# Optimization experiments

Measured on AMD Instinct MI355X. Metric: run time of the kernel, lower is better.

The kernel has to match this reference:

```python
import jax, jax.numpy as jnp
import numpy as np

HID = 512
HEADS = 8
D = HID // HEADS          # att_size = 64
B = 64                    # number of graphs
L = 1024                  # bonds per graph (equal-length scopes)
SCALE = D ** (-0.5)
EPS = 1e-5


def setup_inputs() -> dict:
    key = jax.random.key(0)
    ks = jax.random.split(key, 9)
    f = lambda k, s, sc=1.0: jax.random.normal(k, s, dtype=jnp.float32) * sc
    edge_attr = f(ks[0], (B * L, HID))
    # contiguous equal-length scopes: (start, length) per graph
    scopes = np.stack([np.arange(B, dtype=np.int64) * L,
                       np.full(B, L, dtype=np.int64)], axis=1)
    return {
        "edge_attr": edge_attr,
        "batch_scopes": jnp.asarray(scopes),
        "Wq": f(ks[1], (HID, HID), 0.03),   # torch Linear weight [out, in]
        "Wk": f(ks[2], (HID, HID), 0.03),
        "Wv": f(ks[3], (HID, HID), 0.03),
        "Wr": f(ks[4], (D, D), 0.1),
        "w_alpha": f(ks[5], (D,)),
        "w_beta": f(ks[6], (D,)),
        "Wo": f(ks[7], (HID, HID), 0.03),
        "bo": jnp.zeros((HID,), jnp.float32),
        "ln_g": jnp.ones((HID,), jnp.float32),
        "ln_b": jnp.zeros((HID,), jnp.float32),
    }


def reference(edge_attr, batch_scopes, Wq, Wk, Wv, Wr, w_alpha, w_beta,
              Wo, bo, ln_g, ln_b):
    # Scopes are contiguous, equal length L -> pad_sequence == reshape
    padded = edge_attr.reshape(B, L, HID)

    def proj(W):  # (B, L, HID) @ W.T -> (B, heads, L, D)
        return jnp.einsum('blh,dh->bld', padded, W).reshape(B, L, HEADS, D).transpose(0, 2, 1, 3)

    b_q = proj(Wq)
    b_k = proj(Wk)
    b_v = proj(Wv)

    # softmax over the head-feature dim (faithful to dim=-1 in torch code)
    alpha = jax.nn.softmax(b_q * w_alpha * SCALE, axis=-1)
    global_q = jnp.sum(alpha * b_q, axis=2)            # (B, heads, D), sum over L

    p = global_q[:, :, None, :] * b_k                  # (B, heads, L, D)
    beta = jax.nn.softmax(p * w_beta * SCALE, axis=-1)
    global_k = jnp.sum(beta * p, axis=2)               # (B, heads, D)

    kv = global_k[:, :, None, :] * b_v                 # (B, heads, L, D)
    kv_out = jnp.einsum('bhld,ed->bhle', kv, Wr)
    att = jax.nn.relu(kv_out + b_q)                    # dropout p=0 (eval)

    att = att.transpose(0, 2, 1, 3).reshape(B, L, HID)
    out = jnp.einsum('blh,oh->blo', att, Wo) + bo

    # LayerNorm over last dim
    mu = jnp.mean(out, axis=-1, keepdims=True)
    var = jnp.mean((out - mu) ** 2, axis=-1, keepdims=True)
    out = (out - mu) * jax.lax.rsqrt(var + EPS) * ln_g + ln_b

    # unpad + concat == flatten for equal-length contiguous scopes
    return out.reshape(B * L, HID)
```

## Files before the change

kernel.cpp:

```cpp
#include <hip/hip_runtime.h>
#include <stdint.h>


#define SCALE_F 0.125f
#define EPSF 1e-5f

typedef __attribute__((ext_vector_type(8))) short short8;
typedef __attribute__((ext_vector_type(4))) float float4v;
typedef unsigned short ushort_t;

__device__ __forceinline__ ushort_t f2bf(float f) {
  uint32_t u = __builtin_bit_cast(uint32_t, f);
  u += 0x7fffu + ((u >> 16) & 1u);
  return (ushort_t)(u >> 16);
}
__device__ __forceinline__ float bf2f(ushort_t s) {
  uint32_t u = ((uint32_t)s) << 16;
  return __builtin_bit_cast(float, u);
}

__device__ __forceinline__ void gload16(const void* g, void* l) {
  __builtin_amdgcn_global_load_lds(
      (__attribute__((address_space(1))) char*)(char*)const_cast<void*>(g),
      (__attribute__((address_space(3))) char*)(char*)l, 16, 0, 0);
}

#define BARR() asm volatile("s_barrier" ::: "memory")
#define LGKM0() do { asm volatile("s_waitcnt lgkmcnt(0)" ::: "memory"); \
                     __builtin_amdgcn_sched_barrier(0); } while (0)

__global__ __launch_bounds__(256) void cvt_x(const float* __restrict__ X,
                                             ushort_t* __restrict__ Xb) {
  const int i = blockIdx.x * 256 + threadIdx.x;
  const float4v* src = (const float4v*)X;
  float4v v0 = src[(size_t)i * 2];
  float4v v1 = src[(size_t)i * 2 + 1];
  short8 o;
#pragma unroll
  for (int j = 0; j < 4; ++j) {
    o[j]     = (short)f2bf(v0[j]);
    o[j + 4] = (short)f2bf(v1[j]);
  }
  ((short8*)Xb)[i] = o;
}

__global__ __launch_bounds__(256) void cvt_w(const float* __restrict__ Wq,
                                             const float* __restrict__ Wk,
                                             const float* __restrict__ Wv,
                                             const float* __restrict__ Wo,
                                             ushort_t* __restrict__ Wqkv,
                                             ushort_t* __restrict__ Wob) {
  const int i = blockIdx.x * 256 + threadIdx.x;
  if (i < 262144)        Wqkv[i] = f2bf(Wq[i]);
  else if (i < 524288)   Wqkv[i] = f2bf(Wk[i - 262144]);
  else if (i < 786432)   Wqkv[i] = f2bf(Wv[i - 524288]);
  else                   Wob[i - 786432] = f2bf(Wo[i - 786432]);
}

__global__ __launch_bounds__(512, 2) void gemm8p(const ushort_t* __restrict__ A,
                                                 const ushort_t* __restrict__ Bm,
                                                 ushort_t* __restrict__ C) {
  __shared__ __align__(16) char ldsA[65536];
  __shared__ __align__(16) char ldsB[65536];
  const int swz = (blockIdx.x & 7) * 192 + (blockIdx.x >> 3);
  const int tm = swz / 6, tn = swz % 6;
  const int row0 = tm * 256, col0 = tn * 256;
  const int tid = threadIdx.x, wid = tid >> 6, lane = tid & 63;
  const int wr = wid >> 2, wc = wid & 3;
  const int lr = lane & 15, lk = lane >> 4;
  const int xr = (lr & 7) << 4;

  auto stageA = [&](int kt, int h) {
    const int slot = (2 * kt + h) & 3;
    const int rowbase = row0 + h * 128;
#pragma unroll
    for (int i = 0; i < 2; ++i) {
      const int o = i * 8192 + wid * 1024 + lane * 16;
      const int r = o >> 7, x = o & 127;
      gload16((const char*)A + (size_t)(rowbase + r) * 1024 + kt * 128 + (x ^ ((r & 7) << 4)),
              ldsA + slot * 16384 + i * 8192 + wid * 1024);
    }
  };
  auto stageB = [&](int kt, int h) {
    const int slot = (2 * kt + h) & 3;
    const int rowbase = col0 + h * 128;
#pragma unroll
    for (int i = 0; i < 2; ++i) {
      const int o = i * 8192 + wid * 1024 + lane * 16;
      const int r = o >> 7, x = o & 127;
      gload16((const char*)Bm + (size_t)(rowbase + r) * 1024 + kt * 128 + (x ^ ((r & 7) << 4)),
              ldsB + slot * 16384 + i * 8192 + wid * 1024);
    }
  };
  auto rdA = [&](int t, int mi, int kk) -> short8 {
    const int slot = (2 * t + wr) & 3;
    return *(const short8*)(ldsA + slot * 16384 + (mi * 16 + lr) * 128 +
                            ((kk * 64 + lk * 16) ^ xr));
  };
  auto rdB = [&](int t, int ni, int kk) -> short8 {
    const int slot = (2 * t + (wc >> 1)) & 3;
    return *(const short8*)(ldsB + slot * 16384 + ((wc & 1) * 64 + ni * 16 + lr) * 128 +
                            ((kk * 64 + lk * 16) ^ xr));
  };

  float4v acc[8][4] = {};

  stageA(0, 0); stageA(0, 1); stageB(0, 0); stageB(0, 1);
  stageA(1, 0); stageA(1, 1); stageB(1, 0);
  asm volatile("s_waitcnt vmcnt(6)" ::: "memory");
  BARR();

#pragma unroll
  for (int t = 0; t < 8; ++t) {
    short8 a0[4][2], a1[4][2], b0[2][2], b1[2][2];
#pragma unroll
    for (int mi = 0; mi < 4; ++mi)
#pragma unroll
      for (int kk = 0; kk < 2; ++kk) a0[mi][kk] = rdA(t, mi, kk);
#pragma unroll
    for (int ni = 0; ni < 2; ++ni)
#pragma unroll
      for (int kk = 0; kk < 2; ++kk) b0[ni][kk] = rdB(t, ni, kk);
    if (t + 1 < 8) stageB(t + 1, 1);
    BARR();
    LGKM0();
    __builtin_amdgcn_s_setprio(1);
#pragma unroll
    for (int kk = 0; kk < 2; ++kk)
#pragma unroll
      for (int mi = 0; mi < 4; ++mi)
#pragma unroll
        for (int ni = 0; ni < 2; ++ni)
          acc[mi][ni] = __builtin_amdgcn_mfma_f32_16x16x32_bf16(a0[mi][kk], b0[ni][kk], acc[mi][ni], 0, 0, 0);
    __builtin_amdgcn_s_setprio(0);
    __builtin_amdgcn_sched_barrier(0);
    BARR();
#pragma unroll
    for (int mi = 0; mi < 4; ++mi)
#pragma unroll
      for (int kk = 0; kk < 2; ++kk) a1[mi][kk] = rdA(t, mi + 4, kk);
#pragma unroll
    for (int ni = 0; ni < 2; ++ni)
#pragma unroll
      for (int kk = 0; kk < 2; ++kk) b1[ni][kk] = rdB(t, ni + 2, kk);
    BARR();
    LGKM0();
    __builtin_amdgcn_s_setprio(1);
#pragma unroll
    for (int kk = 0; kk < 2; ++kk)
#pragma unroll
      for (int mi = 0; mi < 4; ++mi)
#pragma unroll
        for (int ni = 0; ni < 2; ++ni)
          acc[mi][ni + 2] = __builtin_amdgcn_mfma_f32_16x16x32_bf16(a0[mi][kk], b1[ni][kk], acc[mi][ni + 2], 0, 0, 0);
    __builtin_amdgcn_s_setprio(0);
    __builtin_amdgcn_sched_barrier(0);
    BARR();
    if (t + 2 < 8) { stageA(t + 2, 0); stageA(t + 2, 1); }
    __builtin_amdgcn_sched_barrier(0);
    __builtin_amdgcn_s_setprio(1);
#pragma unroll
    for (int kk = 0; kk < 2; ++kk)
#pragma unroll
      for (int mi = 0; mi < 4; ++mi)
#pragma unroll
        for (int ni = 0; ni < 2; ++ni)
          acc[mi + 4][ni] = __builtin_amdgcn_mfma_f32_16x16x32_bf16(a1[mi][kk], b0[ni][kk], acc[mi + 4][ni], 0, 0, 0);
    __builtin_amdgcn_s_setprio(0);
    __builtin_amdgcn_sched_barrier(0);
    BARR();
    if (t + 2 < 8) stageB(t + 2, 0);
    __builtin_amdgcn_sched_barrier(0);
    __builtin_amdgcn_s_setprio(1);
#pragma unroll
    for (int kk = 0; kk < 2; ++kk)
#pragma unroll
      for (int mi = 0; mi < 4; ++mi)
#pragma unroll
        for (int ni = 0; ni < 2; ++ni)
          acc[mi + 4][ni + 2] = __builtin_amdgcn_mfma_f32_16x16x32_bf16(a1[mi][kk], b1[ni][kk], acc[mi + 4][ni + 2], 0, 0, 0);
    __builtin_amdgcn_s_setprio(0);
    __builtin_amdgcn_sched_barrier(0);
    if (t < 6) {
      asm volatile("s_waitcnt vmcnt(6)" ::: "memory");
    } else if (t == 6) {
      asm volatile("s_waitcnt vmcnt(0)" ::: "memory");
    }
    BARR();
  }

#pragma unroll
  for (int mi = 0; mi < 8; ++mi)
#pragma unroll
    for (int ni = 0; ni < 4; ++ni) {
      const int col = col0 + wc * 64 + ni * 16 + lr;
#pragma unroll
      for (int r = 0; r < 4; ++r) {
        const int row = row0 + wr * 128 + mi * 16 + lk * 4 + r;
        C[(size_t)row * 1536 + col] = f2bf(acc[mi][ni][r]);
      }
    }
}

__global__ __launch_bounds__(512) void reduce_att(const ushort_t* __restrict__ QKV,
                                                  const float* __restrict__ Wr,
                                                  const float* __restrict__ w_alpha,
                                                  const float* __restrict__ w_beta,
                                                  ushort_t* __restrict__ att) {
  const int bh = blockIdx.x, b = bh >> 3, h = bh & 7;
  const int tid = threadIdx.x, wid = tid >> 6, lane = tid & 63;
  const int rsub = lane >> 3, dch = lane & 7;
  __shared__ float red[8][64];
  __shared__ float gq_s[64];
  __shared__ float gk_s[64];
  __shared__ __align__(16) ushort_t Ml[64 * 72];
  float wa[8], wb[8];
#pragma unroll
  for (int j = 0; j < 8; ++j) {
    wa[j] = w_alpha[dch * 8 + j] * SCALE_F;
    wb[j] = w_beta[dch * 8 + j] * SCALE_F;
  }
  const size_t base = (size_t)b * 1024;
  float acc[8] = {0, 0, 0, 0, 0, 0, 0, 0};
  for (int it = 0; it < 16; ++it) {
    const size_t t = base + it * 64 + wid * 8 + rsub;
    short8 raw = *(const short8*)(QKV + t * 1536 + h * 64 + dch * 8);
    float q[8], s[8];
#pragma unroll
    for (int j = 0; j < 8; ++j) { q[j] = bf2f((ushort_t)raw[j]); s[j] = q[j] * wa[j]; }
    float m = s[0];
#pragma unroll
    for (int j = 1; j < 8; ++j) m = fmaxf(m, s[j]);
    m = fmaxf(m, __shfl_xor(m, 1)); m = fmaxf(m, __shfl_xor(m, 2)); m = fmaxf(m, __shfl_xor(m, 4));
    float e[8], sum = 0.f;
#pragma unroll
    for (int j = 0; j < 8; ++j) { e[j] = __expf(s[j] - m); sum += e[j]; }
    sum += __shfl_xor(sum, 1); sum += __shfl_xor(sum, 2); sum += __shfl_xor(sum, 4);
    const float inv = 1.0f / sum;
#pragma unroll
    for (int j = 0; j < 8; ++j) acc[j] += e[j] * inv * q[j];
  }
#pragma unroll
  for (int msk = 8; msk < 64; msk <<= 1)
#pragma unroll
    for (int j = 0; j < 8; ++j) acc[j] += __shfl_xor(acc[j], msk);
  if (lane < 8) {
#pragma unroll
    for (int j = 0; j < 8; ++j) red[wid][lane * 8 + j] = acc[j];
  }
  __syncthreads();
  if (tid < 64) {
    float s = 0.f;
#pragma unroll
    for (int w = 0; w < 8; ++w) s += red[w][tid];
    gq_s[tid] = s;
  }
  __syncthreads();
  float gq[8];
#pragma unroll
  for (int j = 0; j < 8; ++j) gq[j] = gq_s[dch * 8 + j];
  float gkacc[8] = {0, 0, 0, 0, 0, 0, 0, 0};
  for (int it = 0; it < 16; ++it) {
    const size_t t = base + it * 64 + wid * 8 + rsub;
    short8 raw = *(const short8*)(QKV + t * 1536 + 512 + h * 64 + dch * 8);
    float p[8], s[8];
#pragma unroll
    for (int j = 0; j < 8; ++j) { p[j] = gq[j] * bf2f((ushort_t)raw[j]); s[j] = p[j] * wb[j]; }
    float m = s[0];
#pragma unroll
    for (int j = 1; j < 8; ++j) m = fmaxf(m, s[j]);
    m = fmaxf(m, __shfl_xor(m, 1)); m = fmaxf(m, __shfl_xor(m, 2)); m = fmaxf(m, __shfl_xor(m, 4));
    float e[8], sum = 0.f;
#pragma unroll
    for (int j = 0; j < 8; ++j) { e[j] = __expf(s[j] - m); sum += e[j]; }
    sum += __shfl_xor(sum, 1); sum += __shfl_xor(sum, 2); sum += __shfl_xor(sum, 4);
    const float inv = 1.0f / sum;
#pragma unroll
    for (int j = 0; j < 8; ++j) gkacc[j] += e[j] * inv * p[j];
  }
#pragma unroll
  for (int msk = 8; msk < 64; msk <<= 1)
#pragma unroll
    for (int j = 0; j < 8; ++j) gkacc[j] += __shfl_xor(gkacc[j], msk);
  if (lane < 8) {
#pragma unroll
    for (int j = 0; j < 8; ++j) red[wid][lane * 8 + j] = gkacc[j];
  }
  __syncthreads();
  if (tid < 64) {
    float s = 0.f;
#pragma unroll
    for (int w = 0; w < 8; ++w) s += red[w][tid];
    gk_s[tid] = s;
  }
  __syncthreads();
  for (int i = tid; i < 4096; i += 512) {
    const int e = i >> 6, d = i & 63;
    Ml[e * 72 + d] = f2bf(Wr[i] * gk_s[d]);
  }
  __syncthreads();
  const int lr = lane & 15, lk = lane >> 4;
  short8 bfr[4][2];
#pragma unroll
  for (int ni = 0; ni < 4; ++ni)
#pragma unroll
    for (int ks = 0; ks < 2; ++ks)
      bfr[ni][ks] = *(const short8*)&Ml[(ni * 16 + lr) * 72 + ks * 32 + lk * 8];
  const size_t tw = base + wid * 128;
  for (int c = 0; c < 2; ++c) {
    float4v oacc[4][4] = {};
#pragma unroll
    for (int ks = 0; ks < 2; ++ks) {
      short8 a[4];
#pragma unroll
      for (int mi = 0; mi < 4; ++mi) {
        const size_t t = tw + c * 64 + mi * 16 + lr;
        a[mi] = *(const short8*)(QKV + t * 1536 + 1024 + h * 64 + ks * 32 + lk * 8);
      }
#pragma unroll
      for (int mi = 0; mi < 4; ++mi)
#pragma unroll
        for (int ni = 0; ni < 4; ++ni)
          oacc[mi][ni] = __builtin_amdgcn_mfma_f32_16x16x32_bf16(a[mi], bfr[ni][ks], oacc[mi][ni], 0, 0, 0);
    }
#pragma unroll
    for (int mi = 0; mi < 4; ++mi)
#pragma unroll
      for (int ni = 0; ni < 4; ++ni)
#pragma unroll
        for (int r = 0; r < 4; ++r) {
          const size_t t = tw + c * 64 + mi * 16 + lk * 4 + r;
          const int e = ni * 16 + lr;
          float v = oacc[mi][ni][r] + bf2f(QKV[t * 1536 + h * 64 + e]);
          v = fmaxf(v, 0.0f);
          att[t * 512 + h * 64 + e] = f2bf(v);
        }
  }
}

__global__ __launch_bounds__(512, 2) void gemm_ln(const ushort_t* __restrict__ A,
                                                  const ushort_t* __restrict__ Bm,
                                                  float* __restrict__ out,
                                                  const float* __restrict__ bo,
                                                  const float* __restrict__ lng,
                                                  const float* __restrict__ lnb) {
  __shared__ __align__(16) ushort_t As[2][128 * 32];
  __shared__ __align__(16) ushort_t Bs[2][512 * 32];
  __shared__ float red_s[4][128][2];
  __shared__ float tot_s[128][2];
  const int tid = threadIdx.x, wid = tid >> 6, lane = tid & 63;
  const int wr = wid >> 2, wc = wid & 3;
  const int lr = lane & 15, lk = lane >> 4;
  const int row0 = blockIdx.x * 128;
  float4v acc[4][8] = {};

  const int la = lane * 16;
  const int ar = wid * 16 + (lane >> 2);
  const int acb = (lane & 3) * 16;

  auto stage = [&](int buf, int s) {
    const int k0b = s * 64;
    gload16((const char*)A + (size_t)(row0 + ar) * 1024 + k0b + acb,
            (char*)&As[buf][0] + wid * 1024);
#pragma unroll
    for (int i = 0; i < 4; ++i) {
      const int dst = (wid * 4 + i) * 1024;
      const int br = (dst + la) >> 6;
      const int bcb = la & 63;
      gload16((const char*)Bm + (size_t)br * 1024 + k0b + bcb,
              (char*)&Bs[buf][0] + dst);
    }
  };

  stage(0, 0);
  __syncthreads();
  for (int s = 0; s < 16; ++s) {
    const int buf = s & 1;
    if (s < 15) stage(buf ^ 1, s + 1);
    short8 af[4], bf[8];
#pragma unroll
    for (int mi = 0; mi < 4; ++mi)
      af[mi] = *(const short8*)((const char*)&As[buf][0] + (wr * 64 + mi * 16 + lr) * 64 + lk * 16);
#pragma unroll
    for (int ni = 0; ni < 8; ++ni)
      bf[ni] = *(const short8*)((const char*)&Bs[buf][0] + (wc * 128 + ni * 16 + lr) * 64 + lk * 16);
#pragma unroll
    for (int mi = 0; mi < 4; ++mi)
#pragma unroll
      for (int ni = 0; ni < 8; ++ni)
        acc[mi][ni] = __builtin_amdgcn_mfma_f32_16x16x32_bf16(af[mi], bf[ni], acc[mi][ni], 0, 0, 0);
    __syncthreads();
  }

  float bov[8], gv[8], bv[8];
#pragma unroll
  for (int ni = 0; ni < 8; ++ni) {
    const int c = wc * 128 + ni * 16 + lr;
    bov[ni] = bo[c]; gv[ni] = lng[c]; bv[ni] = lnb[c];
  }
#pragma unroll
  for (int mi = 0; mi < 4; ++mi)
#pragma unroll
    for (int ni = 0; ni < 8; ++ni)
#pragma unroll
      for (int r = 0; r < 4; ++r)
        acc[mi][ni][r] += bov[ni];
#pragma unroll
  for (int mi = 0; mi < 4; ++mi)
#pragma unroll
    for (int r = 0; r < 4; ++r) {
      float s = 0.f, q = 0.f;
#pragma unroll
      for (int ni = 0; ni < 8; ++ni) { const float v = acc[mi][ni][r]; s += v; q += v * v; }
      s += __shfl_xor(s, 1); q += __shfl_xor(q, 1);
      s += __shfl_xor(s, 2); q += __shfl_xor(q, 2);
      s += __shfl_xor(s, 4); q += __shfl_xor(q, 4);
      s += __shfl_xor(s, 8); q += __shfl_xor(q, 8);
      if (lr == 0) {
        const int rb = wr * 64 + mi * 16 + lk * 4 + r;
        red_s[wc][rb][0] = s;
        red_s[wc][rb][1] = q;
      }
    }
  __syncthreads();
  if (tid < 128) {
    tot_s[tid][0] = red_s[0][tid][0] + red_s[1][tid][0] + red_s[2][tid][0] + red_s[3][tid][0];
    tot_s[tid][1] = red_s[0][tid][1] + red_s[1][tid][1] + red_s[2][tid][1] + red_s[3][tid][1];
  }
  __syncthreads();
#pragma unroll
  for (int mi = 0; mi < 4; ++mi)
#pragma unroll
    for (int r = 0; r < 4; ++r) {
      const int rb = wr * 64 + mi * 16 + lk * 4 + r;
      const float mu = tot_s[rb][0] * (1.f / 512.f);
      const float var = tot_s[rb][1] * (1.f / 512.f) - mu * mu;
      const float rs = rsqrtf(var + EPSF);
      float* op = out + (size_t)(row0 + rb) * 512 + wc * 128 + lr;
#pragma unroll
      for (int ni = 0; ni < 8; ++ni)
        op[ni * 16] = (acc[mi][ni][r] - mu) * rs * gv[ni] + bv[ni];
    }
}

extern "C" void kernel_launch(void* const* d_in, const int* in_sizes, int n_in,
                              void* d_out, int out_size, void* d_ws, size_t ws_size,
                              hipStream_t stream) {
  const float* X       = (const float*)d_in[0];
  const float* Wq      = (const float*)d_in[2];
  const float* Wk      = (const float*)d_in[3];
  const float* Wv      = (const float*)d_in[4];
  const float* Wr      = (const float*)d_in[5];
  const float* w_alpha = (const float*)d_in[6];
  const float* w_beta  = (const float*)d_in[7];
  const float* Wo      = (const float*)d_in[8];
  const float* bo      = (const float*)d_in[9];
  const float* ln_g    = (const float*)d_in[10];
  const float* ln_b    = (const float*)d_in[11];

  char* ws = (char*)d_ws;
  ushort_t* Xb   = (ushort_t*)(ws);
  ushort_t* Wqkv = (ushort_t*)(ws + 67108864);
  ushort_t* Wob  = (ushort_t*)(ws + 68681728);
  ushort_t* QKV  = (ushort_t*)(ws + 69206016);
  ushort_t* att  = Xb;
  float* out = (float*)d_out;

  hipLaunchKernelGGL(cvt_x, dim3(16384), dim3(256), 0, stream, X, Xb);
  hipLaunchKernelGGL(cvt_w, dim3(4096), dim3(256), 0, stream, Wq, Wk, Wv, Wo, Wqkv, Wob);
  hipLaunchKernelGGL(gemm8p, dim3(1536), dim3(512), 0, stream, Xb, Wqkv, QKV);
  hipLaunchKernelGGL(reduce_att, dim3(512), dim3(512), 0, stream,
                     QKV, Wr, w_alpha, w_beta, att);
  hipLaunchKernelGGL(gemm_ln, dim3(512), dim3(512), 0, stream,
                     att, Wob, out, bo, ln_g, ln_b);
}
```

Measured before the change: 371.1 us.

## Split reduce_att into three kernels with finer sequence-chunk parallelism

Replaces the single 512-block reduce_att kernel with three kernels (reduce_gq, reduce_gk, att_k). Each uses 2048 blocks that split the 1024-bond sequence into four chunks, with per-chunk partial sums written to workspace and combined in the next kernel. The goal is to fill more CUs during the serial reduction phases. The residual b_q add is folded into the MFMA accumulation by multiplying the Q tile with an identity bf16 matrix, which removes the scalar epilogue load. The cost is two extra kernel launches, recomputing Ml in every chunk block, and double MFMA work in the attention stage.

```diff
diff --git a/kernel.cpp b/kernel.cpp
--- a/kernel.cpp
+++ b/kernel.cpp
@@ -202,28 +202,21 @@
     }
 }
 
-__global__ __launch_bounds__(512) void reduce_att(const ushort_t* __restrict__ QKV,
-                                                  const float* __restrict__ Wr,
-                                                  const float* __restrict__ w_alpha,
-                                                  const float* __restrict__ w_beta,
-                                                  ushort_t* __restrict__ att) {
-  const int bh = blockIdx.x, b = bh >> 3, h = bh & 7;
+__global__ __launch_bounds__(256) void reduce_gq(const ushort_t* __restrict__ QKV,
+                                                 const float* __restrict__ w_alpha,
+                                                 float* __restrict__ gq_part) {
+  const int bx = blockIdx.x, bh = bx >> 2, ch = bx & 3;
+  const int b = bh >> 3, h = bh & 7;
   const int tid = threadIdx.x, wid = tid >> 6, lane = tid & 63;
   const int rsub = lane >> 3, dch = lane & 7;
-  __shared__ float red[8][64];
-  __shared__ float gq_s[64];
-  __shared__ float gk_s[64];
-  __shared__ __align__(16) ushort_t Ml[64 * 72];
-  float wa[8], wb[8];
-#pragma unroll
-  for (int j = 0; j < 8; ++j) {
-    wa[j] = w_alpha[dch * 8 + j] * SCALE_F;
-    wb[j] = w_beta[dch * 8 + j] * SCALE_F;
-  }
-  const size_t base = (size_t)b * 1024;
+  __shared__ float red[4][64];
+  float wa[8];
+#pragma unroll
+  for (int j = 0; j < 8; ++j) wa[j] = w_alpha[dch * 8 + j] * SCALE_F;
+  const size_t base = (size_t)b * 1024 + ch * 256;
   float acc[8] = {0, 0, 0, 0, 0, 0, 0, 0};
-  for (int it = 0; it < 16; ++it) {
-    const size_t t = base + it * 64 + wid * 8 + rsub;
+  for (int it = 0; it < 8; ++it) {
+    const size_t t = base + it * 32 + wid * 8 + rsub;
     short8 raw = *(const short8*)(QKV + t * 1536 + h * 64 + dch * 8);
     float q[8], s[8];
 #pragma unroll
@@ -249,19 +242,37 @@
     for (int j = 0; j < 8; ++j) red[wid][lane * 8 + j] = acc[j];
   }
   __syncthreads();
+  if (tid < 64)
+    gq_part[(size_t)bx * 64 + tid] = red[0][tid] + red[1][tid] + red[2][tid] + red[3][tid];
+}
+
+__global__ __launch_bounds__(256) void reduce_gk(const ushort_t* __restrict__ QKV,
+                                                 const float* __restrict__ w_beta,
+                                                 const float* __restrict__ gq_part,
+                                                 float* __restrict__ gk_part) {
+  const int bx = blockIdx.x, bh = bx >> 2, ch = bx & 3;
+  const int b = bh >> 3, h = bh & 7;
+  const int tid = threadIdx.x, wid = tid >> 6, lane = tid & 63;
+  const int rsub = lane >> 3, dch = lane & 7;
+  __shared__ float red[4][64];
+  __shared__ float gq_s[64];
   if (tid < 64) {
     float s = 0.f;
 #pragma unroll
-    for (int w = 0; w < 8; ++w) s += red[w][tid];
+    for (int c = 0; c < 4; ++c) s += gq_part[(size_t)(bh * 4 + c) * 64 + tid];
     gq_s[tid] = s;
   }
   __syncthreads();
-  float gq[8];
-#pragma unroll
-  for (int j = 0; j < 8; ++j) gq[j] = gq_s[dch * 8 + j];
-  float gkacc[8] = {0, 0, 0, 0, 0, 0, 0, 0};
-  for (int it = 0; it < 16; ++it) {
-    const size_t t = base + it * 64 + wid * 8 + rsub;
+  float wb[8], gq[8];
+#pragma unroll
+  for (int j = 0; j < 8; ++j) {
+    wb[j] = w_beta[dch * 8 + j] * SCALE_F;
+    gq[j] = gq_s[dch * 8 + j];
+  }
+  const size_t base = (size_t)b * 1024 + ch * 256;
+  float acc[8] = {0, 0, 0, 0, 0, 0, 0, 0};
+  for (int it = 0; it < 8; ++it) {
+    const size_t t = base + it * 32 + wid * 8 + rsub;
     short8 raw = *(const short8*)(QKV + t * 1536 + 512 + h * 64 + dch * 8);
     float p[8], s[8];
 #pragma unroll
@@ -276,66 +287,82 @@
     sum += __shfl_xor(sum, 1); sum += __shfl_xor(sum, 2); sum += __shfl_xor(sum, 4);
     const float inv = 1.0f / sum;
 #pragma unroll
-    for (int j = 0; j < 8; ++j) gkacc[j] += e[j] * inv * p[j];
+    for (int j = 0; j < 8; ++j) acc[j] += e[j] * inv * p[j];
   }
 #pragma unroll
   for (int msk = 8; msk < 64; msk <<= 1)
 #pragma unroll
-    for (int j = 0; j < 8; ++j) gkacc[j] += __shfl_xor(gkacc[j], msk);
+    for (int j = 0; j < 8; ++j) acc[j] += __shfl_xor(acc[j], msk);
   if (lane < 8) {
 #pragma unroll
-    for (int j = 0; j < 8; ++j) red[wid][lane * 8 + j] = gkacc[j];
-  }
-  __syncthreads();
+    for (int j = 0; j < 8; ++j) red[wid][lane * 8 + j] = acc[j];
+  }
+  __syncthreads();
+  if (tid < 64)
+    gk_part[(size_t)bx * 64 + tid] = red[0][tid] + red[1][tid] + red[2][tid] + red[3][tid];
+}
+
+__global__ __launch_bounds__(256) void att_k(const ushort_t* __restrict__ QKV,
+                                             const float* __restrict__ Wr,
+                                             const float* __restrict__ gk_part,
+                                             ushort_t* __restrict__ att) {
+  const int bx = blockIdx.x, bh = bx >> 2, tc = bx & 3;
+  const int b = bh >> 3, h = bh & 7;
+  const int tid = threadIdx.x, wid = tid >> 6, lane = tid & 63;
+  __shared__ float gk_s[64];
+  __shared__ __align__(16) ushort_t Ml[64 * 72];
   if (tid < 64) {
     float s = 0.f;
 #pragma unroll
-    for (int w = 0; w < 8; ++w) s += red[w][tid];
+    for (int c = 0; c < 4; ++c) s += gk_part[(size_t)(bh * 4 + c) * 64 + tid];
     gk_s[tid] = s;
   }
   __syncthreads();
-  for (int i = tid; i < 4096; i += 512) {
+  for (int i = tid; i < 4096; i += 256) {
     const int e = i >> 6, d = i & 63;
     Ml[e * 72 + d] = f2bf(Wr[i] * gk_s[d]);
   }
   __syncthreads();
   const int lr = lane & 15, lk = lane >> 4;
-  short8 bfr[4][2];
+  short8 bfr[4][2], bfi[4][2];
 #pragma unroll
   for (int ni = 0; ni < 4; ++ni)
 #pragma unroll
-    for (int ks = 0; ks < 2; ++ks)
+    for (int ks = 0; ks < 2; ++ks) {
       bfr[ni][ks] = *(const short8*)&Ml[(ni * 16 + lr) * 72 + ks * 32 + lk * 8];
-  const size_t tw = base + wid * 128;
-  for (int c = 0; c < 2; ++c) {
-    float4v oacc[4][4] = {};
-#pragma unroll
-    for (int ks = 0; ks < 2; ++ks) {
-      short8 a[4];
-#pragma unroll
-      for (int mi = 0; mi < 4; ++mi) {
-        const size_t t = tw + c * 64 + mi * 16 + lr;
-        a[mi] = *(const short8*)(QKV + t * 1536 + 1024 + h * 64 + ks * 32 + lk * 8);
+#pragma unroll
+      for (int j = 0; j < 8; ++j)
+        bfi[ni][ks][j] = (ni * 16 + lr == ks * 32 + lk * 8 + j) ? (short)0x3F80 : (short)0;
+    }
+  const size_t tw = (size_t)b * 1024 + tc * 256 + wid * 64;
+  float4v oacc[4][4] = {};
+#pragma unroll
+  for (int ks = 0; ks < 2; ++ks) {
+    short8 a[4], aq[4];
+#pragma unroll
+    for (int mi = 0; mi < 4; ++mi) {
+      const size_t t = tw + mi * 16 + lr;
+      a[mi]  = *(const short8*)(QKV + t * 1536 + 1024 + h * 64 + ks * 32 + lk * 8);
+      aq[mi] = *(const short8*)(QKV + t * 1536 +        h * 64 + ks * 32 + lk * 8);
+    }
+#pragma unroll
+    for (int mi = 0; mi < 4; ++mi)
+#pragma unroll
+      for (int ni = 0; ni < 4; ++ni) {
+        oacc[mi][ni] = __builtin_amdgcn_mfma_f32_16x16x32_bf16(a[mi],  bfr[ni][ks], oacc[mi][ni], 0, 0, 0);
+        oacc[mi][ni] = __builtin_amdgcn_mfma_f32_16x16x32_bf16(aq[mi], bfi[ni][ks], oacc[mi][ni], 0, 0, 0);
       }
-#pragma unroll
-      for (int mi = 0; mi < 4; ++mi)
-#pragma unroll
-        for (int ni = 0; ni < 4; ++ni)
-          oacc[mi][ni] = __builtin_amdgcn_mfma_f32_16x16x32_bf16(a[mi], bfr[ni][ks], oacc[mi][ni], 0, 0, 0);
-    }
-#pragma unroll
-    for (int mi = 0; mi < 4; ++mi)
-#pragma unroll
-      for (int ni = 0; ni < 4; ++ni)
-#pragma unroll
-        for (int r = 0; r < 4; ++r) {
-          const size_t t = tw + c * 64 + mi * 16 + lk * 4 + r;
-          const int e = ni * 16 + lr;
-          float v = oacc[mi][ni][r] + bf2f(QKV[t * 1536 + h * 64 + e]);
-          v = fmaxf(v, 0.0f);
-          att[t * 512 + h * 64 + e] = f2bf(v);
-        }
-  }
+  }
+#pragma unroll
+  for (int mi = 0; mi < 4; ++mi)
+#pragma unroll
+    for (int ni = 0; ni < 4; ++ni)
+#pragma unroll
+      for (int r = 0; r < 4; ++r) {
+        const size_t t = tw + mi * 16 + lk * 4 + r;
+        const int e = ni * 16 + lr;
+        att[t * 512 + h * 64 + e] = f2bf(fmaxf(oacc[mi][ni][r], 0.0f));
+      }
 }
 
 __global__ __launch_bounds__(512, 2) void gemm_ln(const ushort_t* __restrict__ A,
@@ -459,18 +486,21 @@
   const float* ln_b    = (const float*)d_in[11];
 
   char* ws = (char*)d_ws;
-  ushort_t* Xb   = (ushort_t*)(ws);
-  ushort_t* Wqkv = (ushort_t*)(ws + 67108864);
-  ushort_t* Wob  = (ushort_t*)(ws + 68681728);
-  ushort_t* QKV  = (ushort_t*)(ws + 69206016);
-  ushort_t* att  = Xb;
+  ushort_t* Xb      = (ushort_t*)(ws);
+  ushort_t* Wqkv    = (ushort_t*)(ws + 67108864);
+  ushort_t* Wob     = (ushort_t*)(ws + 68681728);
+  ushort_t* QKV     = (ushort_t*)(ws + 69206016);
+  float*    gq_part = (float*)(ws + 270532608);
+  float*    gk_part = (float*)(ws + 271056896);
+  ushort_t* att     = Xb;
   float* out = (float*)d_out;
 
   hipLaunchKernelGGL(cvt_x, dim3(16384), dim3(256), 0, stream, X, Xb);
   hipLaunchKernelGGL(cvt_w, dim3(4096), dim3(256), 0, stream, Wq, Wk, Wv, Wo, Wqkv, Wob);
   hipLaunchKernelGGL(gemm8p, dim3(1536), dim3(512), 0, stream, Xb, Wqkv, QKV);
-  hipLaunchKernelGGL(reduce_att, dim3(512), dim3(512), 0, stream,
-                     QKV, Wr, w_alpha, w_beta, att);
+  hipLaunchKernelGGL(reduce_gq, dim3(2048), dim3(256), 0, stream, QKV, w_alpha, gq_part);
+  hipLaunchKernelGGL(reduce_gk, dim3(2048), dim3(256), 0, stream, QKV, w_beta, gq_part, gk_part);
+  hipLaunchKernelGGL(att_k, dim3(2048), dim3(256), 0, stream, QKV, Wr, gk_part, att);
   hipLaunchKernelGGL(gemm_ln, dim3(512), dim3(512), 0, stream,
                      att, Wob, out, bo, ln_g, ln_b);
 }
```

After: 328.8 us. -11.4%, faster.
